# Performance work log

Hardware: AMD Instinct MI355X
Metric: run time of the kernel (lower is better)

The kernel has to match this reference:

```python
import jax, jax.numpy as jnp
import numpy as np

B = 128
C_IN = 1
HID = 256
LAT = 256
NC = 4096
NA = 16
G = 4
DH = 256        # DynamicsModel default hidden_dim
CE = DH // 2    # code/action embed dim
IMG = 64
COMMIT = 0.25
DN = ('NCHW', 'OIHW', 'NCHW')


def conv_s2(x, w, b):
    y = jax.lax.conv_general_dilated(x, w, (2, 2), ((1, 1), (1, 1)), dimension_numbers=DN)
    return y + b[None, :, None, None]


def deconv_s2(x, w, b):
    # torch ConvTranspose2d(k=4, s=2, p=1): flip kernel, swap I/O channels,
    wt = jnp.flip(w, (2, 3)).transpose(1, 0, 2, 3)
    y = jax.lax.conv_general_dilated(x, wt, (1, 1), ((2, 2), (2, 2)),
                                     lhs_dilation=(2, 2), dimension_numbers=DN)
    return y + b[None, :, None, None]


def setup_inputs():
    key = jax.random.key(0)
    ks = iter(jax.random.split(key, 64))

    def W(shape, fan_in):
        return jax.random.normal(next(ks), shape, jnp.float32) * np.float32(1.0 / np.sqrt(fan_in))

    inp = {}
    inp['x'] = jax.random.uniform(next(ks), (B, C_IN, IMG, IMG), jnp.float32)
    inp['x_next'] = jax.random.uniform(next(ks), (B, C_IN, IMG, IMG), jnp.float32)
    inp['action'] = jax.random.randint(next(ks), (B,), 0, NA)
    # encoder Conv2d weights: [out, in, 4, 4]
    inp['enc_w1'] = W((HID, C_IN, 4, 4), C_IN * 16); inp['enc_b1'] = jnp.zeros((HID,), jnp.float32)
    inp['enc_w2'] = W((HID, HID, 4, 4), HID * 16);   inp['enc_b2'] = jnp.zeros((HID,), jnp.float32)
    inp['enc_w3'] = W((HID, HID, 4, 4), HID * 16);   inp['enc_b3'] = jnp.zeros((HID,), jnp.float32)
    inp['enc_w4'] = W((LAT, HID, 4, 4), HID * 16);   inp['enc_b4'] = jnp.zeros((LAT,), jnp.float32)
    # decoder ConvTranspose2d weights: [in, out, 4, 4]
    inp['dec_w1'] = W((LAT, HID, 4, 4), LAT * 4);    inp['dec_b1'] = jnp.zeros((HID,), jnp.float32)
    inp['dec_w2'] = W((HID, HID, 4, 4), HID * 4);    inp['dec_b2'] = jnp.zeros((HID,), jnp.float32)
    inp['dec_w3'] = W((HID, HID, 4, 4), HID * 4);    inp['dec_b3'] = jnp.zeros((HID,), jnp.float32)
    inp['dec_w4'] = W((HID, C_IN, 4, 4), HID * 4);   inp['dec_b4'] = jnp.zeros((C_IN,), jnp.float32)
    inp['codebook'] = jax.random.normal(next(ks), (NC, LAT), jnp.float32)
    inp['code_embed'] = W((NC, CE), CE)
    inp['action_embed'] = W((NA, CE), CE)
    d_in = G * G * CE + CE
    inp['dyn_w1'] = W((d_in, DH), d_in);      inp['dyn_b1'] = jnp.zeros((DH,), jnp.float32)
    inp['dyn_w2'] = W((DH, DH), DH);          inp['dyn_b2'] = jnp.zeros((DH,), jnp.float32)
    inp['dyn_w3'] = W((DH, G * G * NC), DH);  inp['dyn_b3'] = jnp.zeros((G * G * NC,), jnp.float32)
    return inp


def reference(x, x_next, action,
              enc_w1, enc_b1, enc_w2, enc_b2, enc_w3, enc_b3, enc_w4, enc_b4,
              dec_w1, dec_b1, dec_w2, dec_b2, dec_w3, dec_b3, dec_w4, dec_b4,
              codebook, code_embed, action_embed,
              dyn_w1, dyn_b1, dyn_w2, dyn_b2, dyn_w3, dyn_b3):
    relu = jax.nn.relu
    sg = jax.lax.stop_gradient

    cb_sq = jnp.sum(codebook * codebook, axis=1)  # [NC]

    def encode(xi):
        h = relu(conv_s2(xi, enc_w1, enc_b1))
        h = relu(conv_s2(h, enc_w2, enc_b2))
        h = relu(conv_s2(h, enc_w3, enc_b3))
        z = conv_s2(h, enc_w4, enc_b4)                   # [B, LAT, G, G]
        zf = z.transpose(0, 2, 3, 1).reshape(-1, LAT)    # [B*G*G, LAT]
        # squared euclidean distances (argmin identical to cdist argmin)
        d2 = jnp.sum(zf * zf, axis=1, keepdims=True) - 2.0 * (zf @ codebook.T) + cb_sq
        codes = jnp.argmin(d2, axis=-1)                  # [B*G*G]
        zq = codebook[codes]                             # [B*G*G, LAT]
        return zf, zq, codes

    zf, zq, codes_flat = encode(x)
    commitment_loss = jnp.mean((zf - sg(zq)) ** 2)
    codebook_loss = jnp.mean((sg(zf) - zq) ** 2)
    vq_loss = codebook_loss + COMMIT * commitment_loss
    zq_st = zf + sg(zq - zf)                             # straight-through

    zq_grid = zq_st.reshape(-1, G, G, LAT).transpose(0, 3, 1, 2)  # [B, LAT, G, G]
    codes = codes_flat.reshape(-1, G, G)

    # decoder
    h = relu(deconv_s2(zq_grid, dec_w1, dec_b1))
    h = relu(deconv_s2(h, dec_w2, dec_b2))
    h = relu(deconv_s2(h, dec_w3, dec_b3))
    recon = jax.nn.sigmoid(deconv_s2(h, dec_w4, dec_b4))  # [B, 1, 64, 64]

    # dynamics
    ce = code_embed[codes].reshape(codes.shape[0], -1)    # [B, G*G*CE]
    ae = action_embed[action]                             # [B, CE]
    h2 = jnp.concatenate([ce, ae], axis=-1)
    h2 = relu(h2 @ dyn_w1 + dyn_b1)
    h2 = relu(h2 @ dyn_w2 + dyn_b2)
    next_logits = (h2 @ dyn_w3 + dyn_b3).reshape(-1, G, G, NC)

    # next-code target (no grad in original)
    _, _, nc_flat = encode(sg(x_next))
    next_codes_target = nc_flat.reshape(-1, G, G)

    return (recon, codes, commitment_loss, codebook_loss, vq_loss,
            next_logits, next_codes_target)
```

## Files before the change

kernel.cpp:

```cpp
#include <hip/hip_runtime.h>
#include <hip/hip_bf16.h>

typedef _Float16 f16;
typedef f16   f16x8 __attribute__((ext_vector_type(8)));
typedef short s16x8 __attribute__((ext_vector_type(8)));
typedef float f32x4 __attribute__((ext_vector_type(4)));
typedef unsigned short u16;

__device__ __forceinline__ f32x4 mfma_f16(f16x8 a, f16x8 b, f32x4 c){
  return __builtin_amdgcn_mfma_f32_16x16x32_f16(a,b,c,0,0,0);
}
__device__ __forceinline__ f32x4 mfma_bf16(s16x8 a, s16x8 b, f32x4 c){
  return __builtin_amdgcn_mfma_f32_16x16x32_bf16(a,b,c,0,0,0);
}
__device__ __forceinline__ u16 f2bf(float v){
  unsigned u = __float_as_uint(v);
  unsigned r = u + 0x7fffu + ((u>>16)&1u);
  return (u16)(r>>16);
}
__device__ __forceinline__ float bf2f(u16 v){ return __uint_as_float(((unsigned)v)<<16); }

#define N_B 128

#define OUT_RECON 0
#define OUT_CODES 524288
#define OUT_LC    526336
#define OUT_NL    526339
#define OUT_NCT   8914947

#define B_E1H  0ull
#define B_E1L  67108864ull
#define B_ZF   67108864ull
#define B_ZQ4  69206016ull
#define B_ZSQ  70254592ull
#define B_ACC  70287360ull
#define B_CODES 70320128ull
#define B_H1   70385664ull
#define B_H2   70516736ull
#define B_H2B  70647808ull
#define B_E3H  71303168ull
#define B_E3L  75497472ull
#define B_D1   71303168ull
#define B_D2   75497472ull
#define B_EMB  92274688ull
#define B_ZFH  100663296ull
#define B_ZFL  101711872ull
#define B_E2H  134217728ull
#define B_E2L  150994944ull
#define B_DOTS 134217728ull
#define B_WE2H 167772160ull
#define B_WE2L 169869312ull
#define B_WE3H 171966464ull
#define B_WE3L 174063616ull
#define B_WE4H 176160768ull
#define B_WE4L 178257920ull
#define B_WD1  180355072ull
#define B_WD2  182452224ull
#define B_WD3  184549376ull
#define B_CBSQ 186646528ull
#define B_ZERO 186712064ull
#define B_CBH  186712576ull
#define B_CBL  188809728ull

__global__ __launch_bounds__(256) void k_pack_enc(const float* __restrict__ w,
                                                  f16* __restrict__ Wh, f16* __restrict__ Wl){
  int o = blockIdx.x*256 + threadIdx.x;
  int j=o&7, l=(o>>3)&63, n=(o>>9)&15, icc=(o>>13)&7, tap=o>>16;
  int ic = icc*32 + (l>>4)*8 + j, oc = n*16 + (l&15);
  float v = w[((size_t)oc*256+ic)*16 + tap];
  f16 h = (f16)v;
  Wh[o]=h; Wl[o]=(f16)(v-(float)h);
}
__global__ __launch_bounds__(256) void k_pack_dec(const float* __restrict__ w, u16* __restrict__ Wp){
  int o = blockIdx.x*256 + threadIdx.x;
  int j=o&7, l=(o>>3)&63, n=(o>>9)&15, icc=(o>>13)&7, tap=o>>16;
  int ic = icc*32 + (l>>4)*8 + j, oc = n*16 + (l&15);
  Wp[o] = f2bf(w[((size_t)ic*256+oc)*16 + tap]);
}
__global__ __launch_bounds__(256) void k_pack_cb(const float* __restrict__ cb,
                                                 f16* __restrict__ H, f16* __restrict__ L){
  int s = blockIdx.x*256 + threadIdx.x;
  int n = s>>8, k = s&255;
  float v = cb[s];
  int nt = n>>4, lr2 = n&15, icc = k>>5, rr = k&31, lq2 = rr>>3, j = rr&7;
  size_t o = ((size_t)(nt*8+icc)*64 + lq2*16 + lr2)*8 + j;
  f16 h = (f16)v; H[o]=h; L[o]=(f16)(v-(float)h);
}
__global__ __launch_bounds__(256) void k_cbsq(const float* __restrict__ cb, float* __restrict__ cbsq,
                                              float* __restrict__ zg){
  int c = blockIdx.x*256 + threadIdx.x;
  if(blockIdx.x==0 && threadIdx.x<128) zg[threadIdx.x]=0.f;
  const float4* r4 = (const float4*)(cb + (size_t)c*256);
  float s = 0.f;
  for(int k=0;k<64;k++){ float4 v=r4[k]; s += v.x*v.x+v.y*v.y+v.z*v.z+v.w*v.w; }
  cbsq[c] = s;
}

__global__ __launch_bounds__(256) void k_conv1(const float* __restrict__ x, const float* __restrict__ w1,
                                               const float* __restrict__ b1,
                                               f16* __restrict__ Oh, f16* __restrict__ Ol){
  int b = blockIdx.x >> 5, oy = blockIdx.x & 31;
  int oc = threadIdx.x;
  __shared__ float xs[4][68];
  for(int i=threadIdx.x;i<264;i+=256){
    int rr=i/66, cc=i-rr*66;
    int iy=2*oy-1+rr, ix=cc-1;
    float v=0.f;
    if((unsigned)iy<64u && (unsigned)ix<64u) v = x[((size_t)b*64+iy)*64+ix];
    xs[rr][cc]=v;
  }
  __syncthreads();
  float wv[16];
  #pragma unroll
  for(int k=0;k<16;k++) wv[k]=w1[oc*16+k];
  float bv=b1[oc];
  for(int ox=0;ox<32;ox++){
    float acc=bv;
    int c0=2*ox;
    #pragma unroll
    for(int kh=0;kh<4;kh++)
      #pragma unroll
      for(int kw=0;kw<4;kw++) acc += wv[kh*4+kw]*xs[kh][c0+kw];
    float v = fmaxf(acc,0.f);
    f16 h=(f16)v;
    size_t o = (((size_t)b*32+oy)*32+ox)*256+oc;
    Oh[o]=h; Ol[o]=(f16)(v-(float)h);
  }
}

template<int MT, int HIN>
__global__ __launch_bounds__(256,2) void k_conv_v3(
    const f16* __restrict__ Ah, const f16* __restrict__ Al,
    const f16* __restrict__ Wh, const f16* __restrict__ Wl,
    const float* __restrict__ bias, f16* __restrict__ Oh, f16* __restrict__ Ol){
  constexpr int HOUT = HIN/2, HH = HOUT*HOUT;
  constexpr int ROWS = MT*16;
  constexpr int OYS  = ROWS/HOUT;
  static_assert(OYS*HOUT == ROWS, "block must cover whole oy rows");
  constexpr int IYT = 2*OYS + 2;
  constexpr int IXT = HIN + 2;
  constexpr int XS  = 40;
  constexpr int RS  = IXT*XS;
  constexpr int BUF = IYT*RS;
  constexpr int ITEMS = IYT*IXT*8;
  __shared__ f16 As[2*BUF];
  const int tid = threadIdx.x, lane = tid&63, w = tid>>6;
  const int lr = lane&15, lq = lane>>4;
  const int m_base = blockIdx.x*ROWS;
  const int b = m_base/HH;
  const int oy0 = (m_base - b*HH)/HOUT;
  const int iy0 = 2*oy0 - 1;
  const size_t gimg = (size_t)b*HIN*HIN*256;

  int rb[MT];
  #pragma unroll
  for(int t=0;t<MT;t++){
    int r = t*16 + lr;
    int oyl = r/HOUT, oxl = r - oyl*HOUT;
    rb[t] = (2*oyl)*RS + (2*oxl)*XS + lq*8;
  }

  f32x4 acc[MT][4];
  #pragma unroll
  for(int t=0;t<MT;t++)
    #pragma unroll
    for(int u=0;u<4;u++) acc[t][u] = (f32x4){0.f,0.f,0.f,0.f};

  for(int icc=0;icc<8;icc++){
    __syncthreads();
    for(int s=tid;s<ITEMS;s+=256){
      int c = s&7, posi = s>>3;
      int hl = c>>2, ck = c&3;
      int iyl = posi/IXT, ixl = posi - iyl*IXT;
      int iy = iy0 + iyl, ix = ixl - 1;
      f16x8 v = {0,0,0,0,0,0,0,0};
      if((unsigned)iy<(unsigned)HIN && (unsigned)ix<(unsigned)HIN){
        const f16* src = (hl ? Al : Ah) + gimg + (size_t)(iy*HIN+ix)*256 + icc*32 + ck*8;
        v = *(const f16x8*)src;
      }
      *(f16x8*)&As[hl*BUF + iyl*RS + ixl*XS + ck*8] = v;
    }
    __syncthreads();
    #pragma unroll
    for(int th=0;th<4;th++){
      #pragma unroll
      for(int tw=0;tw<4;tw++){
        const int tap = th*4 + tw;
        f16x8 a_h[MT], a_l[MT];
        #pragma unroll
        for(int t=0;t<MT;t++){
          int off = rb[t] + th*RS + tw*XS;
          a_h[t] = *(const f16x8*)&As[off];
          a_l[t] = *(const f16x8*)&As[BUF + off];
        }
        size_t wb = ((size_t)(tap*8+icc)*16 + w*4)*512 + lane*8;
        #pragma unroll
        for(int u=0;u<4;u++){
          f16x8 b_h = *(const f16x8*)(Wh + wb + u*512);
          f16x8 b_l = *(const f16x8*)(Wl + wb + u*512);
          #pragma unroll
          for(int t=0;t<MT;t++){
            acc[t][u] = mfma_f16(a_h[t], b_h, acc[t][u]);
            acc[t][u] = mfma_f16(a_h[t], b_l, acc[t][u]);
            acc[t][u] = mfma_f16(a_l[t], b_h, acc[t][u]);
          }
        }
      }
    }
  }
  #pragma unroll
  for(int t=0;t<MT;t++){
    #pragma unroll
    for(int u=0;u<4;u++){
      int n = (w*4+u)*16 + lr;
      float bv = bias[n];
      #pragma unroll
      for(int r=0;r<4;r++){
        int m = m_base + t*16 + lq*4 + r;
        float v = fmaxf(acc[t][u][r] + bv, 0.f);
        size_t o = (size_t)m*256 + n;
        f16 h=(f16)v; Oh[o]=h; Ol[o]=(f16)(v-(float)h);
      }
    }
  }
}

__global__ __launch_bounds__(512,4) void k_conv_v6(
    const f16* __restrict__ Ah, const f16* __restrict__ Al,
    const f16* __restrict__ Wh, const f16* __restrict__ Wl,
    const float* __restrict__ bias, f16* __restrict__ Oh, f16* __restrict__ Ol){
  constexpr int HIN = 32, HOUT = 16, HH = 256;
  constexpr int ROWS = 64;
  constexpr int IYT = 10, IXT = 34, XS = 40;
  constexpr int RS  = IXT*XS;
  constexpr int BUF = IYT*RS;
  constexpr int ITEMS = IYT*IXT*8;
  __shared__ __align__(16) f16 As[2*BUF];
  const int tid = threadIdx.x, lane = tid&63, w = tid>>6;
  const int wg = w>>2, wn = w&3;
  const int lr = lane&15, lq = lane>>4;
  const int m_base = blockIdx.x*ROWS;
  const int b = m_base/HH;
  const int oy0 = (m_base - b*HH)/HOUT;
  const int iy0 = 2*oy0 - 1;
  const size_t gimg = (size_t)b*HIN*HIN*256;

  int rbw[4];
  #pragma unroll
  for(int t=0;t<4;t++){
    int r = t*16 + lr;
    int oyl = r>>4, oxl = r&15;
    rbw[t] = (2*oyl + 2*wg)*RS + (2*oxl)*XS + lq*8;
  }
  const size_t wgb = (size_t)wg*524288;

  f32x4 acc[4][4];
  #pragma unroll
  for(int t=0;t<4;t++)
    #pragma unroll
    for(int u=0;u<4;u++) acc[t][u] = (f32x4){0.f,0.f,0.f,0.f};

  for(int icc=0;icc<8;icc++){
    __syncthreads();
    for(int s=tid;s<ITEMS;s+=512){
      int c = s&7, posi = s>>3;
      int hl = c>>2, ck = c&3;
      int iyl = posi/IXT, ixl = posi - iyl*IXT;
      int iy = iy0 + iyl, ix = ixl - 1;
      f16x8 v = {0,0,0,0,0,0,0,0};
      if((unsigned)iy<(unsigned)HIN && (unsigned)ix<(unsigned)HIN){
        const f16* src = (hl ? Al : Ah) + gimg + (size_t)(iy*HIN+ix)*256 + icc*32 + ck*8;
        v = *(const f16x8*)src;
      }
      *(f16x8*)&As[hl*BUF + iyl*RS + ixl*XS + ck*8] = v;
    }
    __syncthreads();
    #pragma unroll
    for(int tap8=0;tap8<8;tap8++){
      f16x8 a_h[4], a_l[4];
      #pragma unroll
      for(int t=0;t<4;t++){
        int off = rbw[t] + (tap8>>2)*RS + (tap8&3)*XS;
        a_h[t] = *(const f16x8*)&As[off];
        a_l[t] = *(const f16x8*)&As[BUF + off];
      }
      size_t wb = wgb + ((size_t)(tap8*8+icc)*16 + wn*4)*512 + lane*8;
      #pragma unroll
      for(int u=0;u<4;u++){
        f16x8 b_h = *(const f16x8*)(Wh + wb + u*512);
        f16x8 b_l = *(const f16x8*)(Wl + wb + u*512);
        #pragma unroll
        for(int t=0;t<4;t++){
          acc[t][u] = mfma_f16(a_h[t], b_h, acc[t][u]);
          acc[t][u] = mfma_f16(a_h[t], b_l, acc[t][u]);
          acc[t][u] = mfma_f16(a_l[t], b_h, acc[t][u]);
        }
      }
    }
  }

  float* Rs = (float*)As;
  #pragma unroll
  for(int rr=0;rr<2;rr++){
    __syncthreads();
    if(wg==1){
      #pragma unroll
      for(int t2=0;t2<2;t2++)
        #pragma unroll
        for(int u=0;u<4;u++)
          *(f32x4*)&Rs[((wn*64+lane)*8 + t2*4 + u)*4] = acc[rr*2+t2][u];
    }
    __syncthreads();
    if(wg==0){
      #pragma unroll
      for(int t2=0;t2<2;t2++)
        #pragma unroll
        for(int u=0;u<4;u++){
          f32x4 o = *(const f32x4*)&Rs[((wn*64+lane)*8 + t2*4 + u)*4];
          acc[rr*2+t2][u] += o;
        }
    }
  }
  if(wg==0){
    #pragma unroll
    for(int t=0;t<4;t++){
      #pragma unroll
      for(int u=0;u<4;u++){
        int n = (wn*4+u)*16 + lr;
        float bv = bias[n];
        #pragma unroll
        for(int r=0;r<4;r++){
          int m = m_base + t*16 + lq*4 + r;
          float v = fmaxf(acc[t][u][r] + bv, 0.f);
          size_t o = (size_t)m*256 + n;
          f16 h=(f16)v; Oh[o]=h; Ol[o]=(f16)(v-(float)h);
        }
      }
    }
  }
}

template<int MT>
__global__ __launch_bounds__(256) void k_conv4(
    const f16* __restrict__ Ah, const f16* __restrict__ Al,
    const f16* __restrict__ Wh, const f16* __restrict__ Wl,
    const float* __restrict__ bias, float* __restrict__ Of,
    f16* __restrict__ Zh, f16* __restrict__ Zl,
    const f16* __restrict__ Zp, int Hin){
  const int Hout = Hin>>1, HH = Hout*Hout;
  const int lane = threadIdx.x & 63, w = threadIdx.x >> 6;
  const int lr = lane & 15, lq = lane >> 4;
  const int m_base = blockIdx.x * (16*MT);
  int iyb[MT], ixb[MT], bb[MT];
  #pragma unroll
  for(int t=0;t<MT;t++){
    int m = m_base + t*16 + lr;
    int b = m/HH, rem = m - b*HH;
    int oy = rem/Hout, ox = rem - oy*Hout;
    bb[t]=b; iyb[t]=2*oy-1; ixb[t]=2*ox-1;
  }
  f32x4 acc[MT][4];
  #pragma unroll
  for(int t=0;t<MT;t++)
    #pragma unroll
    for(int u=0;u<4;u++) acc[t][u]=(f32x4){0.f,0.f,0.f,0.f};

  for(int tap=0;tap<16;tap++){
    int th=tap>>2, tw=tap&3;
    const f16* pH[MT]; const f16* pL[MT];
    #pragma unroll
    for(int t=0;t<MT;t++){
      int iy=iyb[t]+th, ix=ixb[t]+tw;
      bool val = ((unsigned)iy<(unsigned)Hin) && ((unsigned)ix<(unsigned)Hin);
      size_t o = (((size_t)bb[t]*Hin+iy)*Hin+ix)*256 + lq*8;
      pH[t] = val ? Ah+o : Zp;
      pL[t] = val ? Al+o : Zp;
    }
    #pragma unroll
    for(int icc=0;icc<8;icc++){
      f16x8 a_h[MT], a_l[MT];
      #pragma unroll
      for(int t=0;t<MT;t++){
        a_h[t] = *(const f16x8*)(pH[t] + icc*32);
        a_l[t] = *(const f16x8*)(pL[t] + icc*32);
      }
      size_t wb = ((size_t)(tap*8+icc)*16 + w*4)*512 + lane*8;
      #pragma unroll
      for(int u=0;u<4;u++){
        f16x8 b_h = *(const f16x8*)(Wh + wb + u*512);
        f16x8 b_l = *(const f16x8*)(Wl + wb + u*512);
        #pragma unroll
        for(int t=0;t<MT;t++){
          acc[t][u] = mfma_f16(a_h[t], b_h, acc[t][u]);
          acc[t][u] = mfma_f16(a_h[t], b_l, acc[t][u]);
          acc[t][u] = mfma_f16(a_l[t], b_h, acc[t][u]);
        }
      }
    }
  }
  #pragma unroll
  for(int t=0;t<MT;t++){
    #pragma unroll
    for(int u=0;u<4;u++){
      int n = (w*4+u)*16 + lr;
      float bv = bias[n];
      #pragma unroll
      for(int r=0;r<4;r++){
        int m = m_base + t*16 + lq*4 + r;
        float v = acc[t][u][r] + bv;
        size_t o = (size_t)m*256 + n;
        Of[o]=v;
        f16 h=(f16)v; Zh[o]=h; Zl[o]=(f16)(v-(float)h);
      }
    }
  }
}

template<int MT>
__global__ __launch_bounds__(256) void k_deconv_mfma(
    const u16* __restrict__ In, const u16* __restrict__ Wp,
    const float* __restrict__ bias, u16* __restrict__ Out,
    const u16* __restrict__ Zp, int H){
  const int Ho = H*2, HH = H*H;
  const int kh = blockIdx.y>>1, kw = blockIdx.y&1;
  const int lane = threadIdx.x & 63, w = threadIdx.x >> 6;
  const int lr = lane & 15, lq = lane >> 4;
  const int m_base = blockIdx.x * (16*MT);
  int jb[MT], ib[MT], bb[MT];
  #pragma unroll
  for(int t=0;t<MT;t++){
    int m = m_base + t*16 + lr;
    int b = m/HH, rem = m - b*HH;
    jb[t]=rem/H; ib[t]=rem-jb[t]*H; bb[t]=b;
  }
  f32x4 acc[MT][4];
  #pragma unroll
  for(int t=0;t<MT;t++)
    #pragma unroll
    for(int u=0;u<4;u++) acc[t][u]=(f32x4){0.f,0.f,0.f,0.f};

  #pragma unroll
  for(int dy=0;dy<2;dy++){
    #pragma unroll
    for(int dx=0;dx<2;dx++){
      int t16 = (kh+2*dy)*4 + (kw+2*dx);
      const u16* pA[MT];
      #pragma unroll
      for(int t=0;t<MT;t++){
        int r = jb[t]+(1-kh)-dy, c = ib[t]+(1-kw)-dx;
        bool val = ((unsigned)r<(unsigned)H) && ((unsigned)c<(unsigned)H);
        size_t o = (((size_t)bb[t]*H+r)*H+c)*256 + lq*8;
        pA[t] = val ? In+o : Zp;
      }
      #pragma unroll
      for(int icc=0;icc<8;icc++){
        s16x8 a[MT];
        #pragma unroll
        for(int t=0;t<MT;t++) a[t] = *(const s16x8*)(pA[t] + icc*32);
        size_t wb = ((size_t)(t16*8+icc)*16 + w*4)*512 + lane*8;
        #pragma unroll
        for(int u=0;u<4;u++){
          s16x8 bfr = *(const s16x8*)(Wp + wb + u*512);
          #pragma unroll
          for(int t=0;t<MT;t++) acc[t][u] = mfma_bf16(a[t], bfr, acc[t][u]);
        }
      }
    }
  }
  #pragma unroll
  for(int t=0;t<MT;t++){
    #pragma unroll
    for(int u=0;u<4;u++){
      int n = (w*4+u)*16 + lr;
      float bv = bias[n];
      #pragma unroll
      for(int r=0;r<4;r++){
        int m = m_base + t*16 + lq*4 + r;
        int b = m/HH, rem = m - b*HH;
        int j = rem/H, i = rem - j*H;
        int oy = 2*j + (1-kh), ox = 2*i + (1-kw);
        float v = fmaxf(acc[t][u][r] + bv, 0.f);
        Out[(((size_t)b*Ho+oy)*Ho+ox)*256 + n] = f2bf(v);
      }
    }
  }
}

__global__ __launch_bounds__(256) void k_dec4(const u16* __restrict__ In, const float* __restrict__ w4,
                                              const float* __restrict__ bias, float* __restrict__ out){
  __shared__ float wt[16][256];
  int t = threadIdx.x;
  for(int i=t;i<4096;i+=256) wt[i&15][i>>4] = w4[i];
  __syncthreads();
  int ox = t & 63, oy = (blockIdx.x<<2) + (t>>6), b = blockIdx.y;
  int iyh=(oy+1)>>1, kh=(oy+1)&1;
  int ixh=(ox+1)>>1, kw=(ox+1)&1;
  float acc = bias[0];
  #pragma unroll
  for(int dy=0;dy<2;dy++){
    int r = iyh-dy;
    if((unsigned)r>=32u) continue;
    #pragma unroll
    for(int dx=0;dx<2;dx++){
      int c = ixh-dx;
      if((unsigned)c>=32u) continue;
      const u16* p = In + (((size_t)b*32+r)*32+c)*256;
      int widx = (kh+2*dy)*4 + kw+2*dx;
      float s=0.f;
      for(int ic=0;ic<256;ic+=8){
        s16x8 vv = *(const s16x8*)(p+ic);
        const float* wr = &wt[widx][ic];
        #pragma unroll
        for(int q=0;q<8;q++) s += bf2f((u16)vv[q])*wr[q];
      }
      acc += s;
    }
  }
  out[(size_t)b*4096 + oy*64 + ox] = 1.f/(1.f+__expf(-acc));
}

__global__ __launch_bounds__(256) void k_zsq(const float* __restrict__ zf, float* __restrict__ zsq){
  int r=blockIdx.x, c=threadIdx.x;
  float v = zf[(size_t)r*256+c];
  __shared__ float red[256];
  red[c]=v*v; __syncthreads();
  for(int s=128;s>0;s>>=1){ if(c<s) red[c]+=red[c+s]; __syncthreads(); }
  if(c==0) zsq[r]=red[0];
}

__global__ __launch_bounds__(256,2) void k_dots(
    const f16* __restrict__ ZH, const f16* __restrict__ ZL,
    const f16* __restrict__ CH, const f16* __restrict__ CL, float* __restrict__ D){
  const int lane = threadIdx.x & 63, w = threadIdx.x >> 6;
  const int lr = lane & 15, lq = lane >> 4;
  const int m_base = blockIdx.y*64, nb = blockIdx.x;
  f32x4 acc[4][4];
  #pragma unroll
  for(int t=0;t<4;t++)
    #pragma unroll
    for(int u=0;u<4;u++) acc[t][u]=(f32x4){0.f,0.f,0.f,0.f};
  #pragma unroll
  for(int icc=0;icc<8;icc++){
    f16x8 ah[4], al[4];
    #pragma unroll
    for(int t=0;t<4;t++){
      size_t o = (size_t)(m_base + t*16 + lr)*256 + lq*8 + icc*32;
      ah[t] = *(const f16x8*)(ZH+o);
      al[t] = *(const f16x8*)(ZL+o);
    }
    #pragma unroll
    for(int u=0;u<4;u++){
      int nt = nb*16 + w*4 + u;
      size_t wb = ((size_t)(nt*8+icc)*64 + lane)*8;
      f16x8 b_h = *(const f16x8*)(CH+wb);
      f16x8 b_l = *(const f16x8*)(CL+wb);
      #pragma unroll
      for(int t=0;t<4;t++){
        acc[t][u] = mfma_f16(ah[t], b_h, acc[t][u]);
        acc[t][u] = mfma_f16(ah[t], b_l, acc[t][u]);
        acc[t][u] = mfma_f16(al[t], b_h, acc[t][u]);
      }
    }
  }
  #pragma unroll
  for(int t=0;t<4;t++)
    #pragma unroll
    for(int u=0;u<4;u++){
      int n = nb*256 + (w*4+u)*16 + lr;
      #pragma unroll
      for(int r=0;r<4;r++){
        int m = m_base + t*16 + lq*4 + r;
        D[(size_t)m*4096 + n] = acc[t][u][r];
      }
    }
}

__global__ __launch_bounds__(256) void k_argmin(const float* __restrict__ dots, const float* __restrict__ zsq,
                                                const float* __restrict__ cbsq, int* __restrict__ codes,
                                                float* __restrict__ out_codes){
  int r = blockIdx.x, t = threadIdx.x;
  float zs = zsq[r];
  float bv = 1e30f; int bi = 0x7fffffff;
  for(int c=t;c<4096;c+=256){
    float d = zs + cbsq[c] - 2.f*dots[(size_t)r*4096+c];
    if(d < bv || (d==bv && c<bi)){ bv=d; bi=c; }
  }
  __shared__ float sv[256]; __shared__ int si[256];
  sv[t]=bv; si[t]=bi; __syncthreads();
  for(int s=128;s>0;s>>=1){
    if(t<s){
      float v2=sv[t+s]; int i2=si[t+s];
      if(v2<sv[t] || (v2==sv[t] && i2<si[t])){ sv[t]=v2; si[t]=i2; }
    }
    __syncthreads();
  }
  if(t==0){ codes[r]=si[0]; out_codes[r]=(float)si[0]; }
}

__global__ void k_zero(float* a){ a[0]=0.f; }

__global__ __launch_bounds__(256) void k_zqloss(const float* __restrict__ zf, const float* __restrict__ cb,
                                                const int* __restrict__ codes, u16* __restrict__ zq4,
                                                float* __restrict__ accum){
  int r = blockIdx.x, c = threadIdx.x;
  int code = codes[r];
  float q = cb[(size_t)code*256 + c];
  float d = zf[(size_t)r*256+c] - q;
  zq4[(size_t)r*256 + c] = f2bf(q);
  __shared__ float red[256];
  red[c]=d*d; __syncthreads();
  for(int s=128;s>0;s>>=1){ if(c<s) red[c]+=red[c+s]; __syncthreads(); }
  if(c==0) atomicAdd(accum, red[0]);
}

__global__ void k_final(const float* __restrict__ accum, float* __restrict__ out){
  if(threadIdx.x==0){
    float L = accum[0]*(1.f/524288.f);
    out[0]=L; out[1]=L; out[2]=1.25f*L;
  }
}

__global__ __launch_bounds__(256) void k_embed(const int* __restrict__ codes, const int* __restrict__ action,
                                               const float* __restrict__ ce, const float* __restrict__ ae,
                                               float* __restrict__ emb){
  int b = blockIdx.x;
  for(int j=threadIdx.x;j<2176;j+=256){
    float v;
    if(j<2048){ int g=j>>7; v = ce[(size_t)codes[b*16+g]*128 + (j&127)]; }
    else      { v = ae[(size_t)action[b]*128 + (j-2048)]; }
    emb[(size_t)b*2176+j]=v;
  }
}

__global__ __launch_bounds__(256) void k_mlp(const float* __restrict__ in, const float* __restrict__ w,
                                             const float* __restrict__ bias, float* __restrict__ out,
                                             u16* __restrict__ outb, int K){
  int b = blockIdx.x, n = threadIdx.x;
  extern __shared__ float row[];
  for(int k=n;k<K;k+=256) row[k]=in[(size_t)b*K+k];
  __syncthreads();
  float acc = bias[n];
  for(int k=0;k<K;k++) acc += row[k]*w[(size_t)k*256+n];
  float v = fmaxf(acc,0.f);
  out[(size_t)b*256+n] = v;
  if(outb) outb[(size_t)b*256+n] = f2bf(v);
}

__global__ __launch_bounds__(256,2) void k_head(const u16* __restrict__ A,
                                                const float* __restrict__ w3,
                                                const float* __restrict__ b3,
                                                float* __restrict__ O){
  __shared__ u16 BS[8*64*8];
  const int tid = threadIdx.x, lane = tid&63, w = tid>>6;
  const int lr = lane&15, lq = lane>>4;
  const int nb = blockIdx.x;
  f32x4 acc[8][2];
  #pragma unroll
  for(int mt=0;mt<8;mt++)
    #pragma unroll
    for(int u=0;u<2;u++) acc[mt][u]=(f32x4){0.f,0.f,0.f,0.f};
  for(int icc=0;icc<8;icc++){
    __syncthreads();
    #pragma unroll
    for(int q=0;q<4;q++){
      int s = tid*16 + q*4;
      int kl = s>>7, nl = s&127;
      float4 v = *(const float4*)(w3 + (size_t)(icc*32+kl)*65536 + (size_t)nb*128 + nl);
      float vv[4] = {v.x,v.y,v.z,v.w};
      int j = kl&7, lqk = kl>>3;
      #pragma unroll
      for(int e=0;e<4;e++){
        int n2 = nl+e, ntl = n2>>4, lr2 = n2&15;
        BS[(ntl*64 + lqk*16 + lr2)*8 + j] = f2bf(vv[e]);
      }
    }
    __syncthreads();
    s16x8 a[8];
    #pragma unroll
    for(int mt=0;mt<8;mt++)
      a[mt] = *(const s16x8*)(A + (size_t)(mt*16+lr)*256 + icc*32 + lq*8);
    #pragma unroll
    for(int u=0;u<2;u++){
      int ntl = w*2+u;
      s16x8 bfr = *(const s16x8*)&BS[((size_t)ntl*64 + lane)*8];
      #pragma unroll
      for(int mt=0;mt<8;mt++) acc[mt][u] = mfma_bf16(a[mt], bfr, acc[mt][u]);
    }
  }
  #pragma unroll
  for(int mt=0;mt<8;mt++)
    #pragma unroll
    for(int u=0;u<2;u++){
      int n = nb*128 + (w*2+u)*16 + lr;
      float bv = b3[n];
      #pragma unroll
      for(int r=0;r<4;r++){
        int m = mt*16 + lq*4 + r;
        O[(size_t)m*65536 + n] = acc[mt][u][r] + bv;
      }
    }
}

extern "C" void kernel_launch(void* const* d_in, const int* in_sizes, int n_in,
                              void* d_out, int out_size, void* d_ws, size_t ws_size,
                              hipStream_t stream){
  (void)in_sizes; (void)n_in; (void)out_size; (void)ws_size;
  const float* x    = (const float*)d_in[0];
  const float* xn   = (const float*)d_in[1];
  const int*   act  = (const int*)  d_in[2];
  const float* ew1=(const float*)d_in[3];  const float* eb1=(const float*)d_in[4];
  const float* ew2=(const float*)d_in[5];  const float* eb2=(const float*)d_in[6];
  const float* ew3=(const float*)d_in[7];  const float* eb3=(const float*)d_in[8];
  const float* ew4=(const float*)d_in[9];  const float* eb4=(const float*)d_in[10];
  const float* dw1=(const float*)d_in[11]; const float* db1=(const float*)d_in[12];
  const float* dw2=(const float*)d_in[13]; const float* db2=(const float*)d_in[14];
  const float* dw3=(const float*)d_in[15]; const float* db3=(const float*)d_in[16];
  const float* dw4=(const float*)d_in[17]; const float* db4=(const float*)d_in[18];
  const float* cbk =(const float*)d_in[19];
  const float* cemb=(const float*)d_in[20];
  const float* aemb=(const float*)d_in[21];
  const float* yw1=(const float*)d_in[22]; const float* yb1=(const float*)d_in[23];
  const float* yw2=(const float*)d_in[24]; const float* yb2=(const float*)d_in[25];
  const float* yw3=(const float*)d_in[26]; const float* yb3=(const float*)d_in[27];
  float* out = (float*)d_out;

  char* wsb = (char*)d_ws;
  f16* E1H=(f16*)(wsb+B_E1H); f16* E1L=(f16*)(wsb+B_E1L);
  f16* E2H=(f16*)(wsb+B_E2H); f16* E2L=(f16*)(wsb+B_E2L);
  f16* E3H=(f16*)(wsb+B_E3H); f16* E3L=(f16*)(wsb+B_E3L);
  float* ZF=(float*)(wsb+B_ZF);
  f16* ZFH=(f16*)(wsb+B_ZFH); f16* ZFL=(f16*)(wsb+B_ZFL);
  u16* ZQ4=(u16*)(wsb+B_ZQ4);
  f16* WE2H=(f16*)(wsb+B_WE2H); f16* WE2L=(f16*)(wsb+B_WE2L);
  f16* WE3H=(f16*)(wsb+B_WE3H); f16* WE3L=(f16*)(wsb+B_WE3L);
  f16* WE4H=(f16*)(wsb+B_WE4H); f16* WE4L=(f16*)(wsb+B_WE4L);
  u16* WD1=(u16*)(wsb+B_WD1); u16* WD2=(u16*)(wsb+B_WD2); u16* WD3=(u16*)(wsb+B_WD3);
  f16* CBH=(f16*)(wsb+B_CBH); f16* CBL=(f16*)(wsb+B_CBL);
  float* ZSQ=(float*)(wsb+B_ZSQ); float* CBSQ=(float*)(wsb+B_CBSQ);
  float* EMB=(float*)(wsb+B_EMB); float* H1=(float*)(wsb+B_H1); float* H2=(float*)(wsb+B_H2);
  u16* H2B=(u16*)(wsb+B_H2B);
  float* ACC=(float*)(wsb+B_ACC); int* CODES=(int*)(wsb+B_CODES);
  float* ZG=(float*)(wsb+B_ZERO);
  const f16* Zf16=(const f16*)ZG; const u16* Zbf=(const u16*)ZG;
  float* DOTS=(float*)(wsb+B_DOTS);
  u16* D1=(u16*)(wsb+B_D1);
  u16* D2=(u16*)(wsb+B_D2);
  u16* D3=(u16*)(wsb+B_E1H);

  k_pack_enc<<<4096,256,0,stream>>>(ew2, WE2H, WE2L);
  k_pack_enc<<<4096,256,0,stream>>>(ew3, WE3H, WE3L);
  k_pack_enc<<<4096,256,0,stream>>>(ew4, WE4H, WE4L);
  k_pack_dec<<<4096,256,0,stream>>>(dw1, WD1);
  k_pack_dec<<<4096,256,0,stream>>>(dw2, WD2);
  k_pack_dec<<<4096,256,0,stream>>>(dw3, WD3);
  k_pack_cb <<<4096,256,0,stream>>>(cbk, CBH, CBL);
  k_cbsq<<<16,256,0,stream>>>(cbk, CBSQ, ZG);

  auto encode = [&](const float* img, float* code_out){
    k_conv1<<<4096,256,0,stream>>>(img, ew1, eb1, E1H, E1L);
    k_conv_v6<<<512,512,0,stream>>>(E1H,E1L, WE2H,WE2L, eb2, E2H,E2L);
    k_conv_v3<1,16><<<512,256,0,stream>>>(E2H,E2L, WE3H,WE3L, eb3, E3H,E3L);
    k_conv4<1><<<128,256,0,stream>>>(E3H,E3L, WE4H,WE4L, eb4, ZF, ZFH, ZFL, Zf16, 8);
    k_zsq<<<2048,256,0,stream>>>(ZF, ZSQ);
    k_dots<<<dim3(16,32),256,0,stream>>>(ZFH, ZFL, CBH, CBL, DOTS);
    k_argmin<<<2048,256,0,stream>>>(DOTS, ZSQ, CBSQ, CODES, code_out);
  };

  encode(x, out+OUT_CODES);
  k_zero<<<1,1,0,stream>>>(ACC);
  k_zqloss<<<2048,256,0,stream>>>(ZF, cbk, CODES, ZQ4, ACC);
  k_final<<<1,64,0,stream>>>(ACC, out+OUT_LC);

  k_deconv_mfma<1><<<dim3(128,4),256,0,stream>>>(ZQ4, WD1, db1, D1, Zbf, 4);
  k_deconv_mfma<4><<<dim3(128,4),256,0,stream>>>(D1,  WD2, db2, D2, Zbf, 8);
  k_deconv_mfma<4><<<dim3(512,4),256,0,stream>>>(D2,  WD3, db3, D3, Zbf, 16);
  k_dec4<<<dim3(16,N_B),256,0,stream>>>(D3, dw4, db4, out+OUT_RECON);

  k_embed<<<N_B,256,0,stream>>>(CODES, act, cemb, aemb, EMB);
  k_mlp<<<N_B,256,2176*4,stream>>>(EMB, yw1, yb1, H1, nullptr, 2176);
  k_mlp<<<N_B,256, 256*4,stream>>>(H1,  yw2, yb2, H2, H2B, 256);
  k_head<<<512,256,0,stream>>>(H2B, yw3, yb3, out+OUT_NL);

  encode(xn, out+OUT_NCT);
}
```

Before: 1.755 ms.

## Split conv2/conv3 kernel-row taps across four wave groups with LDS reduction

The encoder conv2 kernel is widened from 512 to 1024 threads, so each of four wave groups handles one kernel row (4 taps) instead of two groups handling two rows each. Partial accumulators are then summed through shared memory. Conv3 gets a new kernel built the same way: 1024 threads with a 4-way tap split replacing the 256-thread per-block version. The goal is more waves in flight and a shorter serial MFMA chain per wave, paid for with extra LDS reduction passes, more barriers, and higher register pressure under the 1024-thread launch bound.

Result: slower. 5.870 ms (+234.5%).

```diff
diff --git a/kernel.cpp b/kernel.cpp
--- a/kernel.cpp
+++ b/kernel.cpp
@@ -128,104 +128,7 @@
   }
 }
 
-template<int MT, int HIN>
-__global__ __launch_bounds__(256,2) void k_conv_v3(
-    const f16* __restrict__ Ah, const f16* __restrict__ Al,
-    const f16* __restrict__ Wh, const f16* __restrict__ Wl,
-    const float* __restrict__ bias, f16* __restrict__ Oh, f16* __restrict__ Ol){
-  constexpr int HOUT = HIN/2, HH = HOUT*HOUT;
-  constexpr int ROWS = MT*16;
-  constexpr int OYS  = ROWS/HOUT;
-  static_assert(OYS*HOUT == ROWS, "block must cover whole oy rows");
-  constexpr int IYT = 2*OYS + 2;
-  constexpr int IXT = HIN + 2;
-  constexpr int XS  = 40;
-  constexpr int RS  = IXT*XS;
-  constexpr int BUF = IYT*RS;
-  constexpr int ITEMS = IYT*IXT*8;
-  __shared__ f16 As[2*BUF];
-  const int tid = threadIdx.x, lane = tid&63, w = tid>>6;
-  const int lr = lane&15, lq = lane>>4;
-  const int m_base = blockIdx.x*ROWS;
-  const int b = m_base/HH;
-  const int oy0 = (m_base - b*HH)/HOUT;
-  const int iy0 = 2*oy0 - 1;
-  const size_t gimg = (size_t)b*HIN*HIN*256;
-
-  int rb[MT];
-  #pragma unroll
-  for(int t=0;t<MT;t++){
-    int r = t*16 + lr;
-    int oyl = r/HOUT, oxl = r - oyl*HOUT;
-    rb[t] = (2*oyl)*RS + (2*oxl)*XS + lq*8;
-  }
-
-  f32x4 acc[MT][4];
-  #pragma unroll
-  for(int t=0;t<MT;t++)
-    #pragma unroll
-    for(int u=0;u<4;u++) acc[t][u] = (f32x4){0.f,0.f,0.f,0.f};
-
-  for(int icc=0;icc<8;icc++){
-    __syncthreads();
-    for(int s=tid;s<ITEMS;s+=256){
-      int c = s&7, posi = s>>3;
-      int hl = c>>2, ck = c&3;
-      int iyl = posi/IXT, ixl = posi - iyl*IXT;
-      int iy = iy0 + iyl, ix = ixl - 1;
-      f16x8 v = {0,0,0,0,0,0,0,0};
-      if((unsigned)iy<(unsigned)HIN && (unsigned)ix<(unsigned)HIN){
-        const f16* src = (hl ? Al : Ah) + gimg + (size_t)(iy*HIN+ix)*256 + icc*32 + ck*8;
-        v = *(const f16x8*)src;
-      }
-      *(f16x8*)&As[hl*BUF + iyl*RS + ixl*XS + ck*8] = v;
-    }
-    __syncthreads();
-    #pragma unroll
-    for(int th=0;th<4;th++){
-      #pragma unroll
-      for(int tw=0;tw<4;tw++){
-        const int tap = th*4 + tw;
-        f16x8 a_h[MT], a_l[MT];
-        #pragma unroll
-        for(int t=0;t<MT;t++){
-          int off = rb[t] + th*RS + tw*XS;
-          a_h[t] = *(const f16x8*)&As[off];
-          a_l[t] = *(const f16x8*)&As[BUF + off];
-        }
-        size_t wb = ((size_t)(tap*8+icc)*16 + w*4)*512 + lane*8;
-        #pragma unroll
-        for(int u=0;u<4;u++){
-          f16x8 b_h = *(const f16x8*)(Wh + wb + u*512);
-          f16x8 b_l = *(const f16x8*)(Wl + wb + u*512);
-          #pragma unroll
-          for(int t=0;t<MT;t++){
-            acc[t][u] = mfma_f16(a_h[t], b_h, acc[t][u]);
-            acc[t][u] = mfma_f16(a_h[t], b_l, acc[t][u]);
-            acc[t][u] = mfma_f16(a_l[t], b_h, acc[t][u]);
-          }
-        }
-      }
-    }
-  }
-  #pragma unroll
-  for(int t=0;t<MT;t++){
-    #pragma unroll
-    for(int u=0;u<4;u++){
-      int n = (w*4+u)*16 + lr;
-      float bv = bias[n];
-      #pragma unroll
-      for(int r=0;r<4;r++){
-        int m = m_base + t*16 + lq*4 + r;
-        float v = fmaxf(acc[t][u][r] + bv, 0.f);
-        size_t o = (size_t)m*256 + n;
-        f16 h=(f16)v; Oh[o]=h; Ol[o]=(f16)(v-(float)h);
-      }
-    }
-  }
-}
-
-__global__ __launch_bounds__(512,4) void k_conv_v6(
+__global__ __launch_bounds__(1024,8) void k_conv_v7(
     const f16* __restrict__ Ah, const f16* __restrict__ Al,
     const f16* __restrict__ Wh, const f16* __restrict__ Wl,
     const float* __restrict__ bias, f16* __restrict__ Oh, f16* __restrict__ Ol){
@@ -250,9 +153,9 @@
   for(int t=0;t<4;t++){
     int r = t*16 + lr;
     int oyl = r>>4, oxl = r&15;
-    rbw[t] = (2*oyl + 2*wg)*RS + (2*oxl)*XS + lq*8;
-  }
-  const size_t wgb = (size_t)wg*524288;
+    rbw[t] = (2*oyl + wg)*RS + (2*oxl)*XS + lq*8;
+  }
+  const size_t wgb = (size_t)wg*262144;
 
   f32x4 acc[4][4];
   #pragma unroll
@@ -262,7 +165,7 @@
 
   for(int icc=0;icc<8;icc++){
     __syncthreads();
-    for(int s=tid;s<ITEMS;s+=512){
+    for(int s=tid;s<ITEMS;s+=1024){
       int c = s&7, posi = s>>3;
       int hl = c>>2, ck = c&3;
       int iyl = posi/IXT, ixl = posi - iyl*IXT;
@@ -276,15 +179,15 @@
     }
     __syncthreads();
     #pragma unroll
-    for(int tap8=0;tap8<8;tap8++){
+    for(int tw=0;tw<4;tw++){
       f16x8 a_h[4], a_l[4];
       #pragma unroll
       for(int t=0;t<4;t++){
-        int off = rbw[t] + (tap8>>2)*RS + (tap8&3)*XS;
+        int off = rbw[t] + tw*XS;
         a_h[t] = *(const f16x8*)&As[off];
         a_l[t] = *(const f16x8*)&As[BUF + off];
       }
-      size_t wb = wgb + ((size_t)(tap8*8+icc)*16 + wn*4)*512 + lane*8;
+      size_t wb = wgb + ((size_t)(tw*8+icc)*16 + wn*4)*512 + lane*8;
       #pragma unroll
       for(int u=0;u<4;u++){
         f16x8 b_h = *(const f16x8*)(Wh + wb + u*512);
@@ -299,26 +202,22 @@
     }
   }
 
-  float* Rs = (float*)As;
-  #pragma unroll
-  for(int rr=0;rr<2;rr++){
-    __syncthreads();
-    if(wg==1){
-      #pragma unroll
-      for(int t2=0;t2<2;t2++)
+  f32x4* Rs = (f32x4*)As;
+  const int rlane = wn*64 + lane;
+  #pragma unroll
+  for(int mf=0;mf<4;mf++){
+    __syncthreads();
+    if(wg>0){
+      #pragma unroll
+      for(int u=0;u<4;u++) Rs[u*768 + (wg-1)*256 + rlane] = acc[mf][u];
+    }
+    __syncthreads();
+    if(wg==0){
+      #pragma unroll
+      for(int u=0;u<4;u++){
         #pragma unroll
-        for(int u=0;u<4;u++)
-          *(f32x4*)&Rs[((wn*64+lane)*8 + t2*4 + u)*4] = acc[rr*2+t2][u];
-    }
-    __syncthreads();
-    if(wg==0){
-      #pragma unroll
-      for(int t2=0;t2<2;t2++)
-        #pragma unroll
-        for(int u=0;u<4;u++){
-          f32x4 o = *(const f32x4*)&Rs[((wn*64+lane)*8 + t2*4 + u)*4];
-          acc[rr*2+t2][u] += o;
-        }
+        for(int g=0;g<3;g++) acc[mf][u] += Rs[u*768 + g*256 + rlane];
+      }
     }
   }
   if(wg==0){
@@ -335,6 +234,95 @@
           size_t o = (size_t)m*256 + n;
           f16 h=(f16)v; Oh[o]=h; Ol[o]=(f16)(v-(float)h);
         }
+      }
+    }
+  }
+}
+
+__global__ __launch_bounds__(1024,8) void k_conv3_v7(
+    const f16* __restrict__ Ah, const f16* __restrict__ Al,
+    const f16* __restrict__ Wh, const f16* __restrict__ Wl,
+    const float* __restrict__ bias, f16* __restrict__ Oh, f16* __restrict__ Ol){
+  constexpr int HIN = 16, HOUT = 8, HH = 64;
+  constexpr int ROWS = 16;
+  constexpr int IYT = 6, IXT = 18, XS = 40;
+  constexpr int RS  = IXT*XS;
+  constexpr int BUF = IYT*RS;
+  constexpr int ITEMS = IYT*IXT*8;
+  __shared__ __align__(16) f16 As[2*BUF];
+  const int tid = threadIdx.x, lane = tid&63, w = tid>>6;
+  const int wg = w>>2, wn = w&3;
+  const int lr = lane&15, lq = lane>>4;
+  const int m_base = blockIdx.x*ROWS;
+  const int b = m_base/HH;
+  const int oy0 = (m_base - b*HH)/HOUT;
+  const int iy0 = 2*oy0 - 1;
+  const size_t gimg = (size_t)b*HIN*HIN*256;
+
+  const int oyl = lr>>3, oxl = lr&7;
+  const int rb = (2*oyl + wg)*RS + (2*oxl)*XS + lq*8;
+  const size_t wgb = (size_t)wg*262144;
+
+  f32x4 acc[4];
+  #pragma unroll
+  for(int u=0;u<4;u++) acc[u] = (f32x4){0.f,0.f,0.f,0.f};
+
+  for(int icc=0;icc<8;icc++){
+    __syncthreads();
+    if(tid < ITEMS){
+      int s = tid;
+      int c = s&7, posi = s>>3;
+      int hl = c>>2, ck = c&3;
+      int iyl = posi/IXT, ixl = posi - iyl*IXT;
+      int iy = iy0 + iyl, ix = ixl - 1;
+      f16x8 v = {0,0,0,0,0,0,0,0};
+      if((unsigned)iy<(unsigned)HIN && (unsigned)ix<(unsigned)HIN){
+        const f16* src = (hl ? Al : Ah) + gimg + (size_t)(iy*HIN+ix)*256 + icc*32 + ck*8;
+        v = *(const f16x8*)src;
+      }
+      *(f16x8*)&As[hl*BUF + iyl*RS + ixl*XS + ck*8] = v;
+    }
+    __syncthreads();
+    #pragma unroll
+    for(int tw=0;tw<4;tw++){
+      int off = rb + tw*XS;
+      f16x8 a_h = *(const f16x8*)&As[off];
+      f16x8 a_l = *(const f16x8*)&As[BUF + off];
+      size_t wb = wgb + ((size_t)(tw*8+icc)*16 + wn*4)*512 + lane*8;
+      #pragma unroll
+      for(int u=0;u<4;u++){
+        f16x8 b_h = *(const f16x8*)(Wh + wb + u*512);
+        f16x8 b_l = *(const f16x8*)(Wl + wb + u*512);
+        acc[u] = mfma_f16(a_h, b_h, acc[u]);
+        acc[u] = mfma_f16(a_h, b_l, acc[u]);
+        acc[u] = mfma_f16(a_l, b_h, acc[u]);
+      }
+    }
+  }
+
+  f32x4* Rs = (f32x4*)As;
+  const int rlane = wn*64 + lane;
+  #pragma unroll
+  for(int u=0;u<4;u++){
+    __syncthreads();
+    if(wg>0) Rs[(wg-1)*256 + rlane] = acc[u];
+    __syncthreads();
+    if(wg==0){
+      #pragma unroll
+      for(int g=0;g<3;g++) acc[u] += Rs[g*256 + rlane];
+    }
+  }
+  if(wg==0){
+    #pragma unroll
+    for(int u=0;u<4;u++){
+      int n = (wn*4+u)*16 + lr;
+      float bv = bias[n];
+      #pragma unroll
+      for(int r=0;r<4;r++){
+        int m = m_base + lq*4 + r;
+        float v = fmaxf(acc[u][r] + bv, 0.f);
+        size_t o = (size_t)m*256 + n;
+        f16 h=(f16)v; Oh[o]=h; Ol[o]=(f16)(v-(float)h);
       }
     }
   }
@@ -758,8 +746,8 @@
 
   auto encode = [&](const float* img, float* code_out){
     k_conv1<<<4096,256,0,stream>>>(img, ew1, eb1, E1H, E1L);
-    k_conv_v6<<<512,512,0,stream>>>(E1H,E1L, WE2H,WE2L, eb2, E2H,E2L);
-    k_conv_v3<1,16><<<512,256,0,stream>>>(E2H,E2L, WE3H,WE3L, eb3, E3H,E3L);
+    k_conv_v7<<<512,1024,0,stream>>>(E1H,E1L, WE2H,WE2L, eb2, E2H,E2L);
+    k_conv3_v7<<<512,1024,0,stream>>>(E2H,E2L, WE3H,WE3L, eb3, E3H,E3L);
     k_conv4<1><<<128,256,0,stream>>>(E3H,E3L, WE4H,WE4L, eb4, ZF, ZFH, ZFL, Zf16, 8);
     k_zsq<<<2048,256,0,stream>>>(ZF, ZSQ);
     k_dots<<<dim3(16,32),256,0,stream>>>(ZFH, ZFL, CBH, CBL, DOTS);
```
